# Performance work log

Measured on AMD Instinct MI355X. Metric: run time of the kernel, lower is better.

The kernel has to match this reference:

```python
import jax, jax.numpy as jnp
import numpy as np
import math

S, B, D, H = 2048, 2, 1024, 16
DK = D // H

def setup_inputs() -> dict:
    key = jax.random.key(0)
    ks = jax.random.split(key, 32)
    f = lambda k, shape, s=1.0: jax.random.normal(k, shape, dtype=jnp.float32) * s
    inp = {
        'qx': f(ks[0], (S, B, D)),
        'kx': f(ks[1], (S, B, D)),
        'vx': f(ks[2], (S, B, D)),
        'qc': f(ks[3], (S, B, D)),
        'kc': f(ks[4], (S, B, D)),
    }
    w = 1.0 / math.sqrt(D)
    names = ['qx_lin', 'kx_lin', 'vx_lin', 'qc_lin', 'kc_lin', 'out_lin']
    for i, n in enumerate(names):
        inp['W_' + n] = f(ks[5 + 2 * i], (D, D), w)
        inp['b_' + n] = f(ks[6 + 2 * i], (D,), w)
    vnames = ['Vqx', 'Vqc', 'Vkx', 'Vkc']
    for i, n in enumerate(vnames):
        inp['W_' + n] = f(ks[17 + 2 * i], (D, 1), w)
        inp['b_' + n] = f(ks[18 + 2 * i], (1,), w)
    return inp

def _forward(qx, kx, vx, qc, kc,
             W_qx_lin, b_qx_lin, W_kx_lin, b_kx_lin, W_vx_lin, b_vx_lin,
             W_qc_lin, b_qc_lin, W_kc_lin, b_kc_lin, W_out_lin, b_out_lin,
             W_Vqx, b_Vqx, W_Vqc, b_Vqc, W_Vkx, b_Vkx, W_Vkc, b_Vkc):
    # [S,B,D] -> [B,S,D]
    qx = jnp.swapaxes(qx, 0, 1)
    kx = jnp.swapaxes(kx, 0, 1)
    vx = jnp.swapaxes(vx, 0, 1)
    qc = jnp.swapaxes(qc, 0, 1)
    kc = jnp.swapaxes(kc, 0, 1)
    bs = qx.shape[0]

    qx = qx @ W_qx_lin + b_qx_lin
    kx = kx @ W_kx_lin + b_kx_lin
    v = vx @ W_vx_lin + b_vx_lin
    qc = qc @ W_qc_lin + b_qc_lin
    kc = kc @ W_kc_lin + b_kc_lin

    lam_q = jax.nn.sigmoid((qx @ W_Vqx + b_Vqx) + (qc @ W_Vqc + b_Vqc))  # [B,S,1]
    lam_k = jax.nn.sigmoid((kx @ W_Vkx + b_Vkx) + (kc @ W_Vkc + b_Vkc))
    q = (1.0 - lam_q) * qx + lam_q * qc
    k = (1.0 - lam_k) * kx + lam_k * kc

    # [B,S,D] -> [B,H,S,dk]
    q = q.reshape(bs, -1, H, DK).transpose(0, 2, 1, 3)
    k = k.reshape(bs, -1, H, DK).transpose(0, 2, 1, 3)
    v = v.reshape(bs, -1, H, DK).transpose(0, 2, 1, 3)

    scores = jnp.einsum('bhqd,bhkd->bhqk', q, k) / math.sqrt(DK)
    attn = jax.nn.softmax(scores, axis=-1)  # dropout is identity in eval
    ctx = jnp.einsum('bhqk,bhkd->bhqd', attn, v)

    concat = ctx.transpose(0, 2, 1, 3).reshape(bs, -1, D)
    out = concat @ W_out_lin + b_out_lin
    return jnp.swapaxes(out, 0, 1)  # back to [S,B,D]

def reference(qx, kx, vx, qc, kc,
              W_qx_lin, b_qx_lin, W_kx_lin, b_kx_lin, W_vx_lin, b_vx_lin,
              W_qc_lin, b_qc_lin, W_kc_lin, b_kc_lin, W_out_lin, b_out_lin,
              W_Vqx, b_Vqx, W_Vqc, b_Vqc, W_Vkx, b_Vkx, W_Vkc, b_Vkc):
    return _forward(qx, kx, vx, qc, kc,
                    W_qx_lin, b_qx_lin, W_kx_lin, b_kx_lin, W_vx_lin, b_vx_lin,
                    W_qc_lin, b_qc_lin, W_kc_lin, b_kc_lin, W_out_lin, b_out_lin,
                    W_Vqx, b_Vqx, W_Vqc, b_Vqc, W_Vkx, b_Vkx, W_Vkc, b_Vkc)
```

## Files before the change

### kernel.cpp

```cpp
#include <hip/hip_runtime.h>
#include <math.h>

typedef unsigned short u16;
typedef __attribute__((ext_vector_type(8))) short short8;
typedef __attribute__((ext_vector_type(4))) float floatx4;
typedef __attribute__((ext_vector_type(4))) unsigned short ushort4v;

__device__ __forceinline__ u16 f2bf(float f) {
    union { float f; unsigned int u; } v; v.f = f;
    unsigned int r = v.u + 0x7fffu + ((v.u >> 16) & 1u);
    return (u16)(r >> 16);
}
__device__ __forceinline__ unsigned int pk2bf(float a, float b) {
#if __has_builtin(__builtin_amdgcn_cvt_pk_bf16_f32)
    auto r = __builtin_amdgcn_cvt_pk_bf16_f32(a, b);
    union { decltype(r) v; unsigned int u; } cv; cv.v = r; return cv.u;
#else
    return (unsigned int)f2bf(a) | ((unsigned int)f2bf(b) << 16);
#endif
}
__device__ __forceinline__ float fexp2(float x) {
#if __has_builtin(__builtin_amdgcn_exp2f)
    return __builtin_amdgcn_exp2f(x);
#else
    return exp2f(x);
#endif
}

__device__ __forceinline__ void swap32(unsigned int& x0, unsigned int& x1, int lane) {
#if __has_builtin(__builtin_amdgcn_permlane32_swap)
    (void)lane;
    auto r = __builtin_amdgcn_permlane32_swap((int)x0, (int)x1, false, false);
    x0 = (unsigned int)r[0]; x1 = (unsigned int)r[1];
#else
    const bool hi = (lane & 32) != 0;
    const unsigned int s = hi ? x0 : x1;
    const unsigned int rr = (unsigned int)__shfl_xor((int)s, 32, 64);
    const unsigned int n0 = hi ? rr : x0;
    const unsigned int n1 = hi ? x1 : rr;
    x0 = n0; x1 = n1;
#endif
}
__device__ __forceinline__ void swap16(unsigned int& x0, unsigned int& x1, int lane) {
#if __has_builtin(__builtin_amdgcn_permlane16_swap)
    (void)lane;
    auto r = __builtin_amdgcn_permlane16_swap((int)x0, (int)x1, false, false);
    x0 = (unsigned int)r[0]; x1 = (unsigned int)r[1];
#else
    const bool hi = (lane & 16) != 0;
    const unsigned int s = hi ? x0 : x1;
    const unsigned int rr = (unsigned int)__shfl_xor((int)s, 16, 64);
    const unsigned int n0 = hi ? rr : x0;
    const unsigned int n1 = hi ? x1 : rr;
    x0 = n0; x1 = n1;
#endif
}

__device__ __forceinline__ void g2l16(const u16* g, u16* l) {
    __builtin_amdgcn_global_load_lds(
        (const __attribute__((address_space(1))) void*)g,
        (__attribute__((address_space(3))) void*)l, 16, 0, 0);
}

struct WFuseJobs { const float* W[4]; const float* wv[4]; const float* bl[4];
                   float* out[4]; float* bdot; };

__global__ __launch_bounds__(256) void wfuse(WFuseJobs wf) {
    const int z = blockIdx.y;
    const float* W = wf.W[z];
    const float* wv = wf.wv[z];
    float* out = wf.out[z];
    const int t = threadIdx.x;
    const int lane = t & 63, w = t >> 6;
#pragma unroll
    for (int i = 0; i < 4; i++) {
        const int row = blockIdx.x * 16 + w * 4 + i;
        const float* Wr = W + (size_t)row * 1024 + lane * 16;
        const float* vr = wv + lane * 16;
        float p = 0.f;
#pragma unroll
        for (int c = 0; c < 4; c++) {
            const floatx4 a = *(const floatx4*)(Wr + c * 4);
            const floatx4 b = *(const floatx4*)(vr + c * 4);
            p += a[0] * b[0] + a[1] * b[1] + a[2] * b[2] + a[3] * b[3];
        }
#pragma unroll
        for (int m = 1; m <= 32; m <<= 1) p += __shfl_xor(p, m);
        if (lane == 0) out[row] = p;
    }
    if (blockIdx.x == 0) {
        const floatx4 bb = *(const floatx4*)(wf.bl[z] + t * 4);
        const floatx4 vv = *(const floatx4*)(wv + t * 4);
        float p = bb[0] * vv[0] + bb[1] * vv[1] + bb[2] * vv[2] + bb[3] * vv[3];
#pragma unroll
        for (int m = 1; m <= 32; m <<= 1) p += __shfl_xor(p, m);
        __shared__ float red[4];
        if ((t & 63) == 0) red[t >> 6] = p;
        __syncthreads();
        if (t == 0) wf.bdot[z] = red[0] + red[1] + red[2] + red[3];
    }
}

struct GCWJobs {
    const float* xa[3]; const float* xc[3];
    const float* w1[3]; const float* w2[3];
    const float* bdot;
    const float* sA[3]; const float* sB[3];
    float* lamout[3];
    u16* dst[3];
    const float* wsrc[6]; u16* wdst[6]; int wstride[6]; int wkoff[6];
};

__global__ __launch_bounds__(256) void gatewt(GCWJobs gj) {
    __shared__ float tile[32][33];
    const int z = blockIdx.y;
    const int t = threadIdx.x;

    if (z >= 3) {
        const int j = z - 3;
        const float* W = gj.wsrc[j];
        u16* Wt = gj.wdst[j];
        const int stride = gj.wstride[j], koff = gj.wkoff[j];
        const int n0 = (blockIdx.x & 31) * 32, k0 = (blockIdx.x >> 5) * 32;
        const int tx = t & 31, ty = t >> 5;
#pragma unroll
        for (int i = 0; i < 4; i++)
            tile[ty + i * 8][tx] = W[(size_t)(k0 + ty + i * 8) * 1024 + n0 + tx];
        __syncthreads();
#pragma unroll
        for (int i = 0; i < 4; i++)
            Wt[(size_t)(n0 + ty + i * 8) * stride + koff + k0 + tx] = f2bf(tile[tx][ty + i * 8]);
        return;
    }

    const int lane = t & 63, w = t >> 6;
    const int row = blockIdx.x * 4 + w;
    const int e0 = lane * 4;

    if (z == 2) {
#pragma unroll
        for (int c = 0; c < 4; c++) {
            const floatx4 a = *(const floatx4*)(gj.xa[2] + (size_t)row * 1024 + c * 256 + e0);
            ushort4v o;
            const unsigned int lo = pk2bf(a[0], a[1]);
            const unsigned int hi = pk2bf(a[2], a[3]);
            o[0] = (u16)(lo & 0xffff); o[1] = (u16)(lo >> 16);
            o[2] = (u16)(hi & 0xffff); o[3] = (u16)(hi >> 16);
            *(ushort4v*)(gj.dst[2] + (size_t)row * 1024 + c * 256 + e0) = o;
        }
        return;
    }

    floatx4 av[4], cv[4];
    float p = 0.f;
#pragma unroll
    for (int c = 0; c < 4; c++) {
        av[c] = *(const floatx4*)(gj.xa[z] + (size_t)row * 1024 + c * 256 + e0);
        cv[c] = *(const floatx4*)(gj.xc[z] + (size_t)row * 1024 + c * 256 + e0);
        const floatx4 w1 = *(const floatx4*)(gj.w1[z] + c * 256 + e0);
        const floatx4 w2 = *(const floatx4*)(gj.w2[z] + c * 256 + e0);
#pragma unroll
        for (int j = 0; j < 4; j++) p += av[c][j] * w1[j] + cv[c][j] * w2[j];
    }
#pragma unroll
    for (int m = 1; m <= 32; m <<= 1) p += __shfl_xor(p, m);
    const float x = p + gj.bdot[2 * z] + gj.bdot[2 * z + 1]
                  + gj.sA[z][0] + gj.sB[z][0];
    const float lam = 1.f / (1.f + exp2f(-x * 1.44269504f));
    if (lane == 0) gj.lamout[z][row] = lam;
    const float oml = 1.f - lam;

    u16* d = gj.dst[z] + (size_t)row * 2048;
#pragma unroll
    for (int c = 0; c < 4; c++) {
        ushort4v o1, o2;
        {
            const unsigned int lo = pk2bf(oml * av[c][0], oml * av[c][1]);
            const unsigned int hi = pk2bf(oml * av[c][2], oml * av[c][3]);
            o1[0] = (u16)(lo & 0xffff); o1[1] = (u16)(lo >> 16);
            o1[2] = (u16)(hi & 0xffff); o1[3] = (u16)(hi >> 16);
        }
        {
            const unsigned int lo = pk2bf(lam * cv[c][0], lam * cv[c][1]);
            const unsigned int hi = pk2bf(lam * cv[c][2], lam * cv[c][3]);
            o2[0] = (u16)(lo & 0xffff); o2[1] = (u16)(lo >> 16);
            o2[2] = (u16)(hi & 0xffff); o2[3] = (u16)(hi >> 16);
        }
        *(ushort4v*)(d + c * 256 + e0) = o1;
        *(ushort4v*)(d + 1024 + c * 256 + e0) = o2;
    }
}

__global__ __launch_bounds__(256) void vtrans(const u16* __restrict__ V,
                                              u16* __restrict__ Vtg) {
    __shared__ u16 tile[32][34];
    const int bh = blockIdx.z, b = bh >> 4, h = bh & 15;
    const int base = b * 1024 + h * 64;
    const int s0 = blockIdx.x * 32, d0 = blockIdx.y * 32;
    const int tx = threadIdx.x & 31, ty = threadIdx.x >> 5;
#pragma unroll
    for (int i = 0; i < 4; i++)
        tile[ty + i * 8][tx] = V[(size_t)(s0 + ty + i * 8) * 2048 + base + d0 + tx];
    __syncthreads();
#pragma unroll
    for (int i = 0; i < 4; i++)
        Vtg[((size_t)bh * 64 + d0 + ty + i * 8) * 2048 + s0 + tx] = tile[tx][ty + i * 8];
}

struct PJob {
    const u16* A; const u16* Bt; int K;
    const float* biasA; const float* biasC; const float* lam;
    u16* out; float* outf; float scale;
};
struct PJobs { PJob j[4]; };

__global__ __launch_bounds__(256, 3) void projall(PJobs jobs) {
    __shared__ __align__(16) u16 As[2][128 * 32];
    __shared__ __align__(16) u16 Bs[2][128 * 32];
    const int nj = gridDim.z;
    const int bid = blockIdx.x + 8 * (blockIdx.y + 32 * blockIdx.z);
    const int sw = (bid & 7) * (32 * nj) + (bid >> 3);
    const PJob jb = jobs.j[sw >> 8];
    const int K = jb.K;
    const int m0 = ((sw >> 3) & 31) * 128;
    const int n0 = (sw & 7) * 128;
    const int t = threadIdx.x;
    const int lane = t & 63;
    const int wid = t >> 6;
    const int wm = wid >> 1, wn = wid & 1;
    const int qd = lane >> 4, lm = lane & 15;

    const floatx4 zero4 = {0.f, 0.f, 0.f, 0.f};
    floatx4 acc[4][4];
#pragma unroll
    for (int i = 0; i < 4; i++)
#pragma unroll
        for (int j2 = 0; j2 < 4; j2++) acc[i][j2] = zero4;

    const int srow = t >> 2;
    const int su = (t & 3) ^ (srow & 3);
    const u16* Ap = jb.A + (size_t)(m0 + srow) * K + su * 8;
    const u16* Bp = jb.Bt + (size_t)(n0 + srow) * K + su * 8;

#define PSTAGE(BUF, KOFF) do {                                         \
        g2l16(Ap + (KOFF),                   &As[BUF][t * 8]);         \
        g2l16(Ap + (KOFF) + (size_t)64 * K,  &As[BUF][2048 + t * 8]);  \
        g2l16(Bp + (KOFF),                   &Bs[BUF][t * 8]);         \
        g2l16(Bp + (KOFF) + (size_t)64 * K,  &Bs[BUF][2048 + t * 8]);  \
    } while (0)

    PSTAGE(0, 0);
    __syncthreads();
    int cur = 0;
    const int ua = (qd ^ (lm & 3)) << 3;
    for (int k0 = 0; k0 < K; k0 += 32) {
        if (k0 + 32 < K) PSTAGE(cur ^ 1, k0 + 32);

        short8 af[4], bfg[4];
#pragma unroll
        for (int i = 0; i < 4; i++) {
            af[i]  = *(const short8*)&As[cur][(wm * 64 + i * 16 + lm) * 32 + ua];
            bfg[i] = *(const short8*)&Bs[cur][(wn * 64 + i * 16 + lm) * 32 + ua];
        }
#pragma unroll
        for (int i = 0; i < 4; i++)
#pragma unroll
            for (int j2 = 0; j2 < 4; j2++)
                acc[i][j2] = __builtin_amdgcn_mfma_f32_16x16x32_bf16(af[i], bfg[j2], acc[i][j2], 0, 0, 0);

        __syncthreads();
        cur ^= 1;
    }
#undef PSTAGE

#pragma unroll
    for (int i = 0; i < 4; i++) {
        const int mb = m0 + wm * 64 + i * 16 + qd * 4;
        float lamv[4];
        if (jb.lam) {
#pragma unroll
            for (int r = 0; r < 4; r++) lamv[r] = jb.lam[mb + r];
        }
#pragma unroll
        for (int j2 = 0; j2 < 4; j2++) {
            const int col = n0 + wn * 64 + j2 * 16 + lm;
            const float bA = jb.biasA[col];
            if (jb.outf) {
#pragma unroll
                for (int r = 0; r < 4; r++)
                    jb.outf[(size_t)(mb + r) * 1024 + col] = acc[i][j2][r] + bA;
            } else if (jb.lam) {
                const float dB = jb.biasC[col] - bA;
#pragma unroll
                for (int r = 0; r < 4; r++)
                    jb.out[(size_t)(mb + r) * 1024 + col] =
                        f2bf((acc[i][j2][r] + bA + lamv[r] * dB) * jb.scale);
            } else {
#pragma unroll
                for (int r = 0; r < 4; r++)
                    jb.out[(size_t)(mb + r) * 1024 + col] =
                        f2bf((acc[i][j2][r] + bA) * jb.scale);
            }
        }
    }
}

__global__ __launch_bounds__(256, 2) void projout(const u16* __restrict__ A,
                                                  const u16* __restrict__ Bt,
                                                  const float* __restrict__ bias,
                                                  float* __restrict__ C) {
    __shared__ __align__(16) u16 As[2][128 * 32];
    __shared__ __align__(16) u16 Bs[2][64 * 32];
    const int K = 1024;
    const int bid = blockIdx.x;
    const int sw = (bid & 7) * 64 + (bid >> 3);
    const int m0 = (sw >> 4) * 128;
    const int n0 = (sw & 15) * 64;
    const int t = threadIdx.x;
    const int lane = t & 63;
    const int wid = t >> 6;
    const int wm = wid >> 1, wn = wid & 1;
    const int qd = lane >> 4, lm = lane & 15;

    const floatx4 zero4 = {0.f, 0.f, 0.f, 0.f};
    floatx4 acc[4][2];
#pragma unroll
    for (int i = 0; i < 4; i++)
#pragma unroll
        for (int j2 = 0; j2 < 2; j2++) acc[i][j2] = zero4;

    const int srow = t >> 2;
    const int su = (t & 3) ^ (srow & 3);
    const u16* Ap = A + (size_t)(m0 + srow) * K + su * 8;
    const u16* Bp = Bt + (size_t)(n0 + srow) * K + su * 8;

#define OSTG(BUF, KOFF) do {                                           \
        g2l16(Ap + (KOFF),                   &As[BUF][t * 8]);         \
        g2l16(Ap + (KOFF) + (size_t)64 * K,  &As[BUF][2048 + t * 8]);  \
        g2l16(Bp + (KOFF),                   &Bs[BUF][t * 8]);         \
    } while (0)

    OSTG(0, 0);
    __syncthreads();
    int cur = 0;
    const int ua = (qd ^ (lm & 3)) << 3;
    for (int k0 = 0; k0 < K; k0 += 32) {
        if (k0 + 32 < K) OSTG(cur ^ 1, k0 + 32);

        short8 af[4], bfg[2];
#pragma unroll
        for (int i = 0; i < 4; i++)
            af[i] = *(const short8*)&As[cur][(wm * 64 + i * 16 + lm) * 32 + ua];
#pragma unroll
        for (int j2 = 0; j2 < 2; j2++)
            bfg[j2] = *(const short8*)&Bs[cur][(wn * 32 + j2 * 16 + lm) * 32 + ua];
#pragma unroll
        for (int i = 0; i < 4; i++)
#pragma unroll
            for (int j2 = 0; j2 < 2; j2++)
                acc[i][j2] = __builtin_amdgcn_mfma_f32_16x16x32_bf16(af[i], bfg[j2], acc[i][j2], 0, 0, 0);

        __syncthreads();
        cur ^= 1;
    }
#undef OSTG

#pragma unroll
    for (int i = 0; i < 4; i++) {
        const int mb = m0 + wm * 64 + i * 16 + qd * 4;
#pragma unroll
        for (int j2 = 0; j2 < 2; j2++) {
            const int col = n0 + wn * 32 + j2 * 16 + lm;
            const float bv = bias[col];
#pragma unroll
            for (int r = 0; r < 4; r++)
                C[(size_t)(mb + r) * 1024 + col] = acc[i][j2][r] + bv;
        }
    }
}

__global__ __launch_bounds__(256, 4) void attn7(
    const u16* __restrict__ Q, const u16* __restrict__ Kk,
    const u16* __restrict__ Vtg, u16* __restrict__ ctxbf) {
    __shared__ __align__(16) u16 SB[16384];

    const int bid = blockIdx.x + 32 * blockIdx.y;
    const int sw = (bid & 7) * 128 + (bid >> 3);
    const int qt = sw & 31;
    const int bh = sw >> 5;
    const int b = bh >> 4, h = bh & 15;
    const int hb = b * 1024 + h * 64;

    const int t = threadIdx.x, lane = t & 63, w = t >> 6;
    const int qd = lane >> 4, lm = lane & 15;
    const int q0w = qt * 64 + w * 16;

    short8 qf[2];
    {
        const u16* qr = Q + (size_t)(q0w + lm) * 2048 + hb;
        qf[0] = *(const short8*)(qr + qd * 8);
        qf[1] = *(const short8*)(qr + 32 + qd * 8);
    }

    const floatx4 zero4 = {0.f, 0.f, 0.f, 0.f};
    floatx4 ctx[4];
#pragma unroll
    for (int g = 0; g < 4; g++) ctx[g] = zero4;
    floatx4 accL = zero4;

    union { unsigned int u[4]; short8 s; } ov;
    ov.u[0] = ov.u[1] = ov.u[2] = ov.u[3] = 0x3F803F80u;
    const short8 onesb = ov.s;

    const int rl = lane >> 3;
    const int cuz = (lane & 7) ^ rl;
    const u16* kp = Kk + (size_t)(w * 16 + rl) * 2048 + hb + cuz * 8;
    const u16* vp = Vtg + ((size_t)bh * 64 + w * 16 + rl) * 2048 + cuz * 8;
    u16* kd = &SB[(w * 16) * 64];
    u16* vd = &SB[4096 + (w * 16) * 64];

    const int rdA = lm * 64 + ((qd ^ (lm & 7)) << 3);
    const int rdB = rdA ^ 32;

#define STAGE(BUF) do {                                             \
        g2l16(kp,            kd + (BUF) * 8192);                    \
        g2l16(kp + 8 * 2048, kd + (BUF) * 8192 + 8 * 64);           \
        g2l16(vp,            vd + (BUF) * 8192);                    \
        g2l16(vp + 8 * 2048, vd + (BUF) * 8192 + 8 * 64);           \
        kp += 64 * 2048; vp += 64;                                  \
    } while (0)

#define COMPUTE(BUF) do {                                                          \
        short8 pa[2];                                                              \
        _Pragma("unroll")                                                          \
        for (int gp = 0; gp < 2; gp++) {                                           \
            unsigned int pw[2][2];                                                 \
            _Pragma("unroll")                                                      \
            for (int g0 = 0; g0 < 2; g0++) {                                       \
                const int g = gp * 2 + g0;                                         \
                const short8 kf0 = *(const short8*)&SB[(BUF) * 8192 + g * 1024 + rdA]; \
                const short8 kf1 = *(const short8*)&SB[(BUF) * 8192 + g * 1024 + rdB]; \
                floatx4 st = zero4;                                                \
                st = __builtin_amdgcn_mfma_f32_16x16x32_bf16(kf0, qf[0], st, 0, 0, 0); \
                st = __builtin_amdgcn_mfma_f32_16x16x32_bf16(kf1, qf[1], st, 0, 0, 0); \
                const float e0 = fexp2(st[0]), e1 = fexp2(st[1]);                  \
                const float e2 = fexp2(st[2]), e3 = fexp2(st[3]);                  \
                pw[g0][0] = pk2bf(e0, e1);                                         \
                pw[g0][1] = pk2bf(e2, e3);                                         \
            }                                                                      \
            unsigned int a0 = pw[0][0], b0 = pw[1][0];                             \
            unsigned int a1 = pw[0][1], b1 = pw[1][1];                             \
            swap32(a0, b0, lane); swap32(a1, b1, lane);                            \
            swap16(a0, b0, lane); swap16(a1, b1, lane);                            \
            union { unsigned int u[4]; short8 s; } cvv;                            \
            cvv.u[0] = a0; cvv.u[1] = a1; cvv.u[2] = b0; cvv.u[3] = b1;            \
            pa[gp] = cvv.s;                                                        \
        }                                                                          \
        __builtin_amdgcn_s_setprio(1);                                             \
        _Pragma("unroll")                                                          \
        for (int g = 0; g < 4; g++) {                                              \
            const short8 vb0 = *(const short8*)&SB[(BUF) * 8192 + 4096 + g * 1024 + rdA]; \
            const short8 vb1 = *(const short8*)&SB[(BUF) * 8192 + 4096 + g * 1024 + rdB]; \
            ctx[g] = __builtin_amdgcn_mfma_f32_16x16x32_bf16(pa[0], vb0, ctx[g], 0, 0, 0); \
            ctx[g] = __builtin_amdgcn_mfma_f32_16x16x32_bf16(pa[1], vb1, ctx[g], 0, 0, 0); \
        }                                                                          \
        accL = __builtin_amdgcn_mfma_f32_16x16x32_bf16(pa[0], onesb, accL, 0, 0, 0); \
        accL = __builtin_amdgcn_mfma_f32_16x16x32_bf16(pa[1], onesb, accL, 0, 0, 0); \
        __builtin_amdgcn_s_setprio(0);                                             \
    } while (0)

    STAGE(0);
#pragma unroll 1
    for (int it = 0; it < 16; it++) {
        __syncthreads();
        STAGE(1);
        COMPUTE(0);
        __syncthreads();
        if (it < 15) STAGE(0);
        COMPUTE(1);
    }
#undef STAGE
#undef COMPUTE

#pragma unroll
    for (int r = 0; r < 4; r++) {
        const float inv = 1.0f / accL[r];
        const int srow = q0w + qd * 4 + r;
        u16* orow = ctxbf + (size_t)srow * 2048 + hb;
#pragma unroll
        for (int g = 0; g < 4; g++)
            orow[g * 16 + lm] = f2bf(ctx[g][r] * inv);
    }
}

extern "C" void kernel_launch(void* const* d_in, const int* in_sizes, int n_in,
                              void* d_out, int out_size, void* d_ws, size_t ws_size,
                              hipStream_t stream) {
    const float* qx = (const float*)d_in[0];
    const float* kx = (const float*)d_in[1];
    const float* vx = (const float*)d_in[2];
    const float* qc = (const float*)d_in[3];
    const float* kc = (const float*)d_in[4];
    const float* W_qx = (const float*)d_in[5];   const float* b_qx = (const float*)d_in[6];
    const float* W_kx = (const float*)d_in[7];   const float* b_kx = (const float*)d_in[8];
    const float* W_vx = (const float*)d_in[9];   const float* b_vx = (const float*)d_in[10];
    const float* W_qc = (const float*)d_in[11];  const float* b_qc = (const float*)d_in[12];
    const float* W_kc = (const float*)d_in[13];  const float* b_kc = (const float*)d_in[14];
    const float* W_out = (const float*)d_in[15]; const float* b_out = (const float*)d_in[16];
    const float* W_Vqx = (const float*)d_in[17]; const float* b_Vqx = (const float*)d_in[18];
    const float* W_Vqc = (const float*)d_in[19]; const float* b_Vqc = (const float*)d_in[20];
    const float* W_Vkx = (const float*)d_in[21]; const float* b_Vkx = (const float*)d_in[22];
    const float* W_Vkc = (const float*)d_in[23]; const float* b_Vkc = (const float*)d_in[24];

    char* ws = (char*)d_ws;
    const size_t MB = 1048576;
    u16* Aq  = (u16*)ws;
    u16* Ak  = (u16*)(ws + 16 * MB);
    u16* Av  = (u16*)(ws + 32 * MB);
    u16* Wtq = (u16*)(ws + 40 * MB);
    u16* Wtk = (u16*)(ws + 44 * MB);
    u16* Wtv = (u16*)(ws + 48 * MB);
    u16* Wto = (u16*)(ws + 50 * MB);
    u16* Pv    = (u16*)(ws + 52 * MB);
    u16* qg    = (u16*)(ws + 60 * MB);
    u16* kg    = (u16*)(ws + 68 * MB);
    u16* ctxbf = (u16*)(ws + 76 * MB);
    float* wfused = (float*)(ws + 84 * MB);
    float* bdot   = (float*)(ws + 84 * MB + 16384);
    float* lam    = (float*)(ws + 84 * MB + 16384 + 256);
    u16* Vtg    = (u16*)(ws + 32 * MB);

    WFuseJobs wf;
    wf.W[0] = W_qx; wf.wv[0] = W_Vqx; wf.bl[0] = b_qx; wf.out[0] = wfused;
    wf.W[1] = W_qc; wf.wv[1] = W_Vqc; wf.bl[1] = b_qc; wf.out[1] = wfused + 1024;
    wf.W[2] = W_kx; wf.wv[2] = W_Vkx; wf.bl[2] = b_kx; wf.out[2] = wfused + 2048;
    wf.W[3] = W_kc; wf.wv[3] = W_Vkc; wf.bl[3] = b_kc; wf.out[3] = wfused + 3072;
    wf.bdot = bdot;
    wfuse<<<dim3(64, 4), 256, 0, stream>>>(wf);

    GCWJobs gj;
    gj.xa[0] = qx; gj.xc[0] = qc; gj.w1[0] = wfused;        gj.w2[0] = wfused + 1024;
    gj.sA[0] = b_Vqx; gj.sB[0] = b_Vqc; gj.lamout[0] = lam;        gj.dst[0] = Aq;
    gj.xa[1] = kx; gj.xc[1] = kc; gj.w1[1] = wfused + 2048; gj.w2[1] = wfused + 3072;
    gj.sA[1] = b_Vkx; gj.sB[1] = b_Vkc; gj.lamout[1] = lam + 4096; gj.dst[1] = Ak;
    gj.xa[2] = vx; gj.xc[2] = nullptr; gj.w1[2] = nullptr; gj.w2[2] = nullptr;
    gj.sA[2] = nullptr; gj.sB[2] = nullptr; gj.lamout[2] = nullptr; gj.dst[2] = Av;
    gj.bdot = bdot;
    gj.wsrc[0] = W_qx; gj.wdst[0] = Wtq; gj.wstride[0] = 2048; gj.wkoff[0] = 0;
    gj.wsrc[1] = W_qc; gj.wdst[1] = Wtq; gj.wstride[1] = 2048; gj.wkoff[1] = 1024;
    gj.wsrc[2] = W_kx; gj.wdst[2] = Wtk; gj.wstride[2] = 2048; gj.wkoff[2] = 0;
    gj.wsrc[3] = W_kc; gj.wdst[3] = Wtk; gj.wstride[3] = 2048; gj.wkoff[3] = 1024;
    gj.wsrc[4] = W_vx; gj.wdst[4] = Wtv; gj.wstride[4] = 1024; gj.wkoff[4] = 0;
    gj.wsrc[5] = W_out; gj.wdst[5] = Wto; gj.wstride[5] = 1024; gj.wkoff[5] = 0;
    gatewt<<<dim3(1024, 9), 256, 0, stream>>>(gj);

    const float QSCALE = 0.18033688011112042f;
    PJobs pj;
    pj.j[0].A = Aq; pj.j[0].Bt = Wtq; pj.j[0].K = 2048;
    pj.j[0].biasA = b_qx; pj.j[0].biasC = b_qc; pj.j[0].lam = lam;
    pj.j[0].out = qg; pj.j[0].outf = nullptr; pj.j[0].scale = QSCALE;
    pj.j[1].A = Ak; pj.j[1].Bt = Wtk; pj.j[1].K = 2048;
    pj.j[1].biasA = b_kx; pj.j[1].biasC = b_kc; pj.j[1].lam = lam + 4096;
    pj.j[1].out = kg; pj.j[1].outf = nullptr; pj.j[1].scale = 1.0f;
    pj.j[2].A = Av; pj.j[2].Bt = Wtv; pj.j[2].K = 1024;
    pj.j[2].biasA = b_vx; pj.j[2].biasC = nullptr; pj.j[2].lam = nullptr;
    pj.j[2].out = Pv; pj.j[2].outf = nullptr; pj.j[2].scale = 1.0f;
    pj.j[3] = pj.j[2];
    projall<<<dim3(8, 32, 3), 256, 0, stream>>>(pj);

    vtrans<<<dim3(64, 2, 32), 256, 0, stream>>>(Pv, Vtg);

    attn7<<<dim3(32, 32), 256, 0, stream>>>(qg, kg, Vtg, ctxbf);

    projout<<<dim3(512), 256, 0, stream>>>(ctxbf, Wto, b_out, (float*)d_out);
}
```

Baseline: 332.4 us.

## Double query rows per warp in attention to reuse K/V tiles

Each warp of the attention kernel now handles 32 query rows (two 16-row groups) instead of 16, so each block covers 128 queries and the grid is halved. Every K and V fragment read from shared memory feeds twice as many MFMAs, which halves LDS and global traffic per unit of work. The cost is roughly double the accumulator registers, launch bounds lowered to 2 blocks per SM, and only 512 blocks, which reduces occupancy and latency hiding.

```diff
diff --git a/kernel.cpp b/kernel.cpp
--- a/kernel.cpp
+++ b/kernel.cpp
@@ -379,34 +379,38 @@
     }
 }
 
-__global__ __launch_bounds__(256, 4) void attn7(
+__global__ __launch_bounds__(256, 2) void attn9(
     const u16* __restrict__ Q, const u16* __restrict__ Kk,
     const u16* __restrict__ Vtg, u16* __restrict__ ctxbf) {
     __shared__ __align__(16) u16 SB[16384];
 
-    const int bid = blockIdx.x + 32 * blockIdx.y;
-    const int sw = (bid & 7) * 128 + (bid >> 3);
-    const int qt = sw & 31;
-    const int bh = sw >> 5;
+    const int bid = blockIdx.x + 16 * blockIdx.y;
+    const int sw = (bid & 7) * 64 + (bid >> 3);
+    const int qt = sw & 15;
+    const int bh = sw >> 4;
     const int b = bh >> 4, h = bh & 15;
     const int hb = b * 1024 + h * 64;
 
     const int t = threadIdx.x, lane = t & 63, w = t >> 6;
     const int qd = lane >> 4, lm = lane & 15;
-    const int q0w = qt * 64 + w * 16;
-
-    short8 qf[2];
-    {
-        const u16* qr = Q + (size_t)(q0w + lm) * 2048 + hb;
-        qf[0] = *(const short8*)(qr + qd * 8);
-        qf[1] = *(const short8*)(qr + 32 + qd * 8);
+    const int q0w = qt * 128 + w * 32;
+
+    short8 qf[2][2];
+#pragma unroll
+    for (int qh = 0; qh < 2; qh++) {
+        const u16* qr = Q + (size_t)(q0w + qh * 16 + lm) * 2048 + hb;
+#pragma unroll
+        for (int c = 0; c < 2; c++)
+            qf[qh][c] = *(const short8*)(qr + c * 32 + qd * 8);
     }
 
     const floatx4 zero4 = {0.f, 0.f, 0.f, 0.f};
-    floatx4 ctx[4];
-#pragma unroll
-    for (int g = 0; g < 4; g++) ctx[g] = zero4;
-    floatx4 accL = zero4;
+    floatx4 ctx[2][4];
+#pragma unroll
+    for (int qh = 0; qh < 2; qh++)
+#pragma unroll
+        for (int g = 0; g < 4; g++) ctx[qh][g] = zero4;
+    floatx4 accL[2] = {zero4, zero4};
 
     union { unsigned int u[4]; short8 s; } ov;
     ov.u[0] = ov.u[1] = ov.u[2] = ov.u[3] = 0x3F803F80u;
@@ -431,41 +435,53 @@
     } while (0)
 
 #define COMPUTE(BUF) do {                                                          \
-        short8 pa[2];                                                              \
+        short8 pa[2][2];                                                           \
         _Pragma("unroll")                                                          \
         for (int gp = 0; gp < 2; gp++) {                                           \
-            unsigned int pw[2][2];                                                 \
+            unsigned int pw[2][2][2];                                              \
             _Pragma("unroll")                                                      \
             for (int g0 = 0; g0 < 2; g0++) {                                       \
                 const int g = gp * 2 + g0;                                         \
                 const short8 kf0 = *(const short8*)&SB[(BUF) * 8192 + g * 1024 + rdA]; \
                 const short8 kf1 = *(const short8*)&SB[(BUF) * 8192 + g * 1024 + rdB]; \
-                floatx4 st = zero4;                                                \
-                st = __builtin_amdgcn_mfma_f32_16x16x32_bf16(kf0, qf[0], st, 0, 0, 0); \
-                st = __builtin_amdgcn_mfma_f32_16x16x32_bf16(kf1, qf[1], st, 0, 0, 0); \
-                const float e0 = fexp2(st[0]), e1 = fexp2(st[1]);                  \
-                const float e2 = fexp2(st[2]), e3 = fexp2(st[3]);                  \
-                pw[g0][0] = pk2bf(e0, e1);                                         \
-                pw[g0][1] = pk2bf(e2, e3);                                         \
+                _Pragma("unroll")                                                  \
+                for (int qh = 0; qh < 2; qh++) {                                   \
+                    floatx4 st = zero4;                                            \
+                    st = __builtin_amdgcn_mfma_f32_16x16x32_bf16(kf0, qf[qh][0], st, 0, 0, 0); \
+                    st = __builtin_amdgcn_mfma_f32_16x16x32_bf16(kf1, qf[qh][1], st, 0, 0, 0); \
+                    const float e0 = fexp2(st[0]), e1 = fexp2(st[1]);              \
+                    const float e2 = fexp2(st[2]), e3 = fexp2(st[3]);              \
+                    pw[qh][g0][0] = pk2bf(e0, e1);                                 \
+                    pw[qh][g0][1] = pk2bf(e2, e3);                                 \
+                }                                                                  \
             }                                                                      \
-            unsigned int a0 = pw[0][0], b0 = pw[1][0];                             \
-            unsigned int a1 = pw[0][1], b1 = pw[1][1];                             \
-            swap32(a0, b0, lane); swap32(a1, b1, lane);                            \
-            swap16(a0, b0, lane); swap16(a1, b1, lane);                            \
-            union { unsigned int u[4]; short8 s; } cvv;                            \
-            cvv.u[0] = a0; cvv.u[1] = a1; cvv.u[2] = b0; cvv.u[3] = b1;            \
-            pa[gp] = cvv.s;                                                        \
+            _Pragma("unroll")                                                      \
+            for (int qh = 0; qh < 2; qh++) {                                       \
+                unsigned int a0 = pw[qh][0][0], b0 = pw[qh][1][0];                 \
+                unsigned int a1 = pw[qh][0][1], b1 = pw[qh][1][1];                 \
+                swap32(a0, b0, lane); swap32(a1, b1, lane);                        \
+                swap16(a0, b0, lane); swap16(a1, b1, lane);                        \
+                union { unsigned int u[4]; short8 s; } cvv;                        \
+                cvv.u[0] = a0; cvv.u[1] = a1; cvv.u[2] = b0; cvv.u[3] = b1;        \
+                pa[qh][gp] = cvv.s;                                                \
+            }                                                                      \
         }                                                                          \
         __builtin_amdgcn_s_setprio(1);                                             \
         _Pragma("unroll")                                                          \
         for (int g = 0; g < 4; g++) {                                              \
             const short8 vb0 = *(const short8*)&SB[(BUF) * 8192 + 4096 + g * 1024 + rdA]; \
             const short8 vb1 = *(const short8*)&SB[(BUF) * 8192 + 4096 + g * 1024 + rdB]; \
-            ctx[g] = __builtin_amdgcn_mfma_f32_16x16x32_bf16(pa[0], vb0, ctx[g], 0, 0, 0); \
-            ctx[g] = __builtin_amdgcn_mfma_f32_16x16x32_bf16(pa[1], vb1, ctx[g], 0, 0, 0); \
+            _Pragma("unroll")                                                      \
+            for (int qh = 0; qh < 2; qh++) {                                       \
+                ctx[qh][g] = __builtin_amdgcn_mfma_f32_16x16x32_bf16(pa[qh][0], vb0, ctx[qh][g], 0, 0, 0); \
+                ctx[qh][g] = __builtin_amdgcn_mfma_f32_16x16x32_bf16(pa[qh][1], vb1, ctx[qh][g], 0, 0, 0); \
+            }                                                                      \
         }                                                                          \
-        accL = __builtin_amdgcn_mfma_f32_16x16x32_bf16(pa[0], onesb, accL, 0, 0, 0); \
-        accL = __builtin_amdgcn_mfma_f32_16x16x32_bf16(pa[1], onesb, accL, 0, 0, 0); \
+        _Pragma("unroll")                                                          \
+        for (int qh = 0; qh < 2; qh++) {                                           \
+            accL[qh] = __builtin_amdgcn_mfma_f32_16x16x32_bf16(pa[qh][0], onesb, accL[qh], 0, 0, 0); \
+            accL[qh] = __builtin_amdgcn_mfma_f32_16x16x32_bf16(pa[qh][1], onesb, accL[qh], 0, 0, 0); \
+        }                                                                          \
         __builtin_amdgcn_s_setprio(0);                                             \
     } while (0)
 
@@ -483,13 +499,16 @@
 #undef COMPUTE
 
 #pragma unroll
-    for (int r = 0; r < 4; r++) {
-        const float inv = 1.0f / accL[r];
-        const int srow = q0w + qd * 4 + r;
-        u16* orow = ctxbf + (size_t)srow * 2048 + hb;
-#pragma unroll
-        for (int g = 0; g < 4; g++)
-            orow[g * 16 + lm] = f2bf(ctx[g][r] * inv);
+    for (int qh = 0; qh < 2; qh++) {
+#pragma unroll
+        for (int r = 0; r < 4; r++) {
+            const float inv = 1.0f / accL[qh][r];
+            const int srow = q0w + qh * 16 + qd * 4 + r;
+            u16* orow = ctxbf + (size_t)srow * 2048 + hb;
+#pragma unroll
+            for (int g = 0; g < 4; g++)
+                orow[g * 16 + lm] = f2bf(ctx[qh][g][r] * inv);
+        }
     }
 }
 
@@ -570,7 +589,7 @@
 
     vtrans<<<dim3(64, 2, 32), 256, 0, stream>>>(Pv, Vtg);
 
-    attn7<<<dim3(32, 32), 256, 0, stream>>>(qg, kg, Vtg, ctxbf);
+    attn9<<<dim3(16, 32), 256, 0, stream>>>(qg, kg, Vtg, ctxbf);
 
     projout<<<dim3(512), 256, 0, stream>>>(ctxbf, Wto, b_out, (float*)d_out);
 }
```

Measured after the change: 321.1 us. 1.04x faster.
